# Optimization experiments

Hardware: AMD Instinct MI355X
Metric: run time of the kernel (lower is better)

## Reference

```python
import jax, jax.numpy as jnp
import numpy as np

B = 65536

def setup_inputs() -> dict:
    key = jax.random.key(0)
    k1, k2 = jax.random.split(key, 2)
    x = jax.random.normal(k1, (B, 1, 28, 28), dtype=jnp.float32)
    # classifier params: Linear(4*14*14 -> 10)
    W = jax.random.normal(k2, (10, 4 * 14 * 14), dtype=jnp.float32) * 0.03
    b = jnp.zeros((10,), dtype=jnp.float32)
    return {"x": x, "W": W, "b": b}


def reference(x, W, b):
    # x: [B,1,28,28]
    batch = x.shape[0]
    img = x[:, 0]  # [B,28,28]
    # non-overlapping 2x2 patches, row-major over (r,c), flattened row-major
    # within patch -> matches torch's x[:, r:r+2, c:c+2].view(B, -1)
    patches = img.reshape(batch, 14, 2, 14, 2).transpose(0, 1, 3, 2, 4)
    patches = patches.reshape(batch, 196, 4)
    # Exact closed form of the 4-qubit circuit RY(theta_i) on wire i followed
    # by CNOT chain (0->1->2->3) and <Z_k> measurement:
    #   <Z_k> = prod_{j<=k} cos(theta_j)
    ez = jnp.cumprod(jnp.cos(patches), axis=-1)  # [B,196,4]
    feat = ez.reshape(batch, 4 * 14 * 14)  # [B,784]
    logits = feat @ W.T + b  # [B,10]
    return jax.nn.log_softmax(logits, axis=-1)
```

## Files before the change

### kernel.cpp

```cpp
#include <hip/hip_runtime.h>

#define NCLS 10
#define NUM_IMG 65536

__device__ __forceinline__ void async_cp16(const float* g, float* l) {
    __builtin_amdgcn_global_load_lds(
        (const __attribute__((address_space(1))) void*)(g),
        (__attribute__((address_space(3))) void*)(l),
        16, 0, 0);
}

__global__ __launch_bounds__(448, 7) void quanv_logits_kernel(
    const float* __restrict__ x,
    const float* __restrict__ W,
    const float* __restrict__ bias,
    float* __restrict__ out)
{
    __shared__ float4 sb[2][896];

    const int tid  = threadIdx.x;
    const int w    = __builtin_amdgcn_readfirstlane(tid >> 6);
    const int lane = tid & 63;
    const int img0 = blockIdx.x << 6;

    const int s0 = tid, s1 = tid + 448;
    const float* g0 = x + (size_t)(img0 + s0 / 14) * 784 + (s0 % 14) * 4;
    const float* g1 = x + (size_t)(img0 + s1 / 14) * 784 + (s1 % 14) * 4;

    float acc[NCLS];
#pragma unroll
    for (int c = 0; c < NCLS; ++c) acc[c] = 0.0f;

    async_cp16(g0, (float*)&sb[0][s0]);
    async_cp16(g1, (float*)&sb[0][s1]);
    __syncthreads();

#pragma unroll
    for (int rr = 0; rr < 14; ++rr) {
        const int cur = rr & 1, nxt = cur ^ 1;
        if (rr < 13) {
            async_cp16(g0 + (rr + 1) * 56, (float*)&sb[nxt][s0]);
            async_cp16(g1 + (rr + 1) * 56, (float*)&sb[nxt][s1]);
        }

        const float4 t4 = sb[cur][lane * 14 + w];
        const float4 b4 = sb[cur][lane * 14 + w + 7];

        const float e0 = __cosf(t4.x);
        const float e1 = e0 * __cosf(t4.y);
        const float e2 = e1 * __cosf(b4.x);
        const float e3 = e2 * __cosf(b4.y);
        const float f0 = __cosf(t4.z);
        const float f1 = f0 * __cosf(t4.w);
        const float f2 = f1 * __cosf(b4.z);
        const float f3 = f2 * __cosf(b4.w);

        const int P = (rr * 14 + 2 * w) * 4;
#pragma unroll
        for (int c = 0; c < NCLS; ++c) {
            const float4 wa = *reinterpret_cast<const float4*>(&W[c * 784 + P]);
            const float4 wb = *reinterpret_cast<const float4*>(&W[c * 784 + P + 4]);
            float a = acc[c];
            a = fmaf(e0, wa.x, a); a = fmaf(e1, wa.y, a);
            a = fmaf(e2, wa.z, a); a = fmaf(e3, wa.w, a);
            a = fmaf(f0, wb.x, a); a = fmaf(f1, wb.y, a);
            a = fmaf(f2, wb.z, a); a = fmaf(f3, wb.w, a);
            acc[c] = a;
        }
        __syncthreads();
    }

    float* part = (float*)sb;
#pragma unroll
    for (int c = 0; c < NCLS; ++c) part[lane * 71 + w * NCLS + c] = acc[c];
    __syncthreads();

    if (w == 0) {
        float s[NCLS];
#pragma unroll
        for (int c = 0; c < NCLS; ++c) s[c] = bias[c];
        for (int ww = 0; ww < 7; ++ww) {
#pragma unroll
            for (int c = 0; c < NCLS; ++c) s[c] += part[lane * 71 + ww * NCLS + c];
        }
        float m = s[0];
#pragma unroll
        for (int c = 1; c < NCLS; ++c) m = fmaxf(m, s[c]);
        float sum = 0.0f;
#pragma unroll
        for (int c = 0; c < NCLS; ++c) sum += __expf(s[c] - m);
        const float lse = __logf(sum) + m;

        float* o = out + (size_t)(img0 + lane) * NCLS;
#pragma unroll
        for (int c = 0; c < NCLS; c += 2) {
            float2 v;
            v.x = s[c]     - lse;
            v.y = s[c + 1] - lse;
            *reinterpret_cast<float2*>(o + c) = v;
        }
    }
}

extern "C" void kernel_launch(void* const* d_in, const int* in_sizes, int n_in,
                              void* d_out, int out_size, void* d_ws, size_t ws_size,
                              hipStream_t stream) {
    const float* x    = (const float*)d_in[0];
    const float* W    = (const float*)d_in[1];
    const float* bias = (const float*)d_in[2];
    float* out        = (float*)d_out;

    dim3 block(448);
    dim3 grid(NUM_IMG / 64);
    quanv_logits_kernel<<<grid, block, 0, stream>>>(x, W, bias, out);
}
```

Baseline: 309.0 us.

## Compute classifier GEMM with bf16 MFMA instead of scalar FMAs

Replaces the per-thread FP32 FMA loop over 10 classes with 16x16x32 bf16 MFMA instructions. Each wave handles 16 images, and the weights are repacked into bf16 fragments in LDS once per block. Image data is now loaded directly from global memory into registers, replacing the double-buffered async LDS copy and its per-row barriers. This removes most scalar FMA work and barrier overhead. In exchange it pays a per-block weight repack, wastes MFMA columns on padding, and lowers precision to bf16.

```diff
diff --git a/kernel.cpp b/kernel.cpp
--- a/kernel.cpp
+++ b/kernel.cpp
@@ -1,88 +1,120 @@
 #include <hip/hip_runtime.h>
+#include <hip/hip_bf16.h>
 
 #define NCLS 10
 #define NUM_IMG 65536
 
-__device__ __forceinline__ void async_cp16(const float* g, float* l) {
-    __builtin_amdgcn_global_load_lds(
-        (const __attribute__((address_space(1))) void*)(g),
-        (__attribute__((address_space(3))) void*)(l),
-        16, 0, 0);
+typedef __attribute__((ext_vector_type(8))) short short8;
+typedef __attribute__((ext_vector_type(4))) float f32x4;
+
+union FragAB { short8 v; unsigned int u[4]; };
+
+__device__ __forceinline__ unsigned int pack_bf16(float a, float b) {
+    union { __hip_bfloat162 h; unsigned int u; } cv;
+    cv.h = __float22bfloat162_rn(make_float2(a, b));
+    return cv.u;
 }
 
-__global__ __launch_bounds__(448, 7) void quanv_logits_kernel(
+__global__ __launch_bounds__(256, 4) void quanv_mfma_kernel(
     const float* __restrict__ x,
     const float* __restrict__ W,
     const float* __restrict__ bias,
     float* __restrict__ out)
 {
-    __shared__ float4 sb[2][896];
+    __shared__ unsigned int sWB[28 * 64 * 4];
+    __shared__ float part[4 * 16 * 18];
 
     const int tid  = threadIdx.x;
-    const int w    = __builtin_amdgcn_readfirstlane(tid >> 6);
+    const int wv   = tid >> 6;
     const int lane = tid & 63;
+    const int q    = lane >> 4;
+    const int sub  = lane & 15;
     const int img0 = blockIdx.x << 6;
 
-    const int s0 = tid, s1 = tid + 448;
-    const float* g0 = x + (size_t)(img0 + s0 / 14) * 784 + (s0 % 14) * 4;
-    const float* g1 = x + (size_t)(img0 + s1 / 14) * 784 + (s1 % 14) * 4;
+    for (int f = tid; f < 28 * 64; f += 256) {
+        const int step = f >> 6, sl = f & 63;
+        const int qB = sl >> 4, n = sl & 15;
+        const int rr = step >> 1, h = step & 1;
+        unsigned int u0 = 0, u1 = 0, u2 = 0, u3 = 0;
+        if (n < NCLS) {
+            const int pr0 = 8 * h + 2 * qB;
+            if (pr0 < 14) {
+                const float* wp = W + n * 784 + (rr * 14 + pr0) * 4;
+                u0 = pack_bf16(wp[0], wp[1]);
+                u1 = pack_bf16(wp[2], wp[3]);
+            }
+            if (pr0 + 1 < 14) {
+                const float* wp = W + n * 784 + (rr * 14 + pr0 + 1) * 4;
+                u2 = pack_bf16(wp[0], wp[1]);
+                u3 = pack_bf16(wp[2], wp[3]);
+            }
+        }
+        *reinterpret_cast<uint4*>(&sWB[f * 4]) = make_uint4(u0, u1, u2, u3);
+    }
+    __syncthreads();
 
-    float acc[NCLS];
-#pragma unroll
-    for (int c = 0; c < NCLS; ++c) acc[c] = 0.0f;
-
-    async_cp16(g0, (float*)&sb[0][s0]);
-    async_cp16(g1, (float*)&sb[0][s1]);
-    __syncthreads();
+    const float* __restrict__ img = x + (size_t)(img0 + wv * 16 + sub) * 784;
+    f32x4 acc = {0.f, 0.f, 0.f, 0.f};
 
 #pragma unroll
     for (int rr = 0; rr < 14; ++rr) {
-        const int cur = rr & 1, nxt = cur ^ 1;
-        if (rr < 13) {
-            async_cp16(g0 + (rr + 1) * 56, (float*)&sb[nxt][s0]);
-            async_cp16(g1 + (rr + 1) * 56, (float*)&sb[nxt][s1]);
+        {
+            const float4 t4 = *reinterpret_cast<const float4*>(img + rr * 56 + q * 4);
+            const float4 b4 = *reinterpret_cast<const float4*>(img + rr * 56 + 28 + q * 4);
+            const float e0 = __cosf(t4.x);
+            const float e1 = e0 * __cosf(t4.y);
+            const float e2 = e1 * __cosf(b4.x);
+            const float e3 = e2 * __cosf(b4.y);
+            const float f0 = __cosf(t4.z);
+            const float f1 = f0 * __cosf(t4.w);
+            const float f2 = f1 * __cosf(b4.z);
+            const float f3 = f2 * __cosf(b4.w);
+            FragAB a;
+            a.u[0] = pack_bf16(e0, e1); a.u[1] = pack_bf16(e2, e3);
+            a.u[2] = pack_bf16(f0, f1); a.u[3] = pack_bf16(f2, f3);
+            FragAB bfr;
+            *reinterpret_cast<uint4*>(bfr.u) =
+                *reinterpret_cast<const uint4*>(&sWB[((rr * 2) * 64 + lane) * 4]);
+            acc = __builtin_amdgcn_mfma_f32_16x16x32_bf16(a.v, bfr.v, acc, 0, 0, 0);
         }
-
-        const float4 t4 = sb[cur][lane * 14 + w];
-        const float4 b4 = sb[cur][lane * 14 + w + 7];
-
-        const float e0 = __cosf(t4.x);
-        const float e1 = e0 * __cosf(t4.y);
-        const float e2 = e1 * __cosf(b4.x);
-        const float e3 = e2 * __cosf(b4.y);
-        const float f0 = __cosf(t4.z);
-        const float f1 = f0 * __cosf(t4.w);
-        const float f2 = f1 * __cosf(b4.z);
-        const float f3 = f2 * __cosf(b4.w);
-
-        const int P = (rr * 14 + 2 * w) * 4;
-#pragma unroll
-        for (int c = 0; c < NCLS; ++c) {
-            const float4 wa = *reinterpret_cast<const float4*>(&W[c * 784 + P]);
-            const float4 wb = *reinterpret_cast<const float4*>(&W[c * 784 + P + 4]);
-            float a = acc[c];
-            a = fmaf(e0, wa.x, a); a = fmaf(e1, wa.y, a);
-            a = fmaf(e2, wa.z, a); a = fmaf(e3, wa.w, a);
-            a = fmaf(f0, wb.x, a); a = fmaf(f1, wb.y, a);
-            a = fmaf(f2, wb.z, a); a = fmaf(f3, wb.w, a);
-            acc[c] = a;
+        {
+            float4 t4 = {0.f, 0.f, 0.f, 0.f}, b4 = {0.f, 0.f, 0.f, 0.f};
+            if (q < 3) {
+                t4 = *reinterpret_cast<const float4*>(img + rr * 56 + 16 + q * 4);
+                b4 = *reinterpret_cast<const float4*>(img + rr * 56 + 44 + q * 4);
+            }
+            const float e0 = __cosf(t4.x);
+            const float e1 = e0 * __cosf(t4.y);
+            const float e2 = e1 * __cosf(b4.x);
+            const float e3 = e2 * __cosf(b4.y);
+            const float f0 = __cosf(t4.z);
+            const float f1 = f0 * __cosf(t4.w);
+            const float f2 = f1 * __cosf(b4.z);
+            const float f3 = f2 * __cosf(b4.w);
+            FragAB a;
+            a.u[0] = pack_bf16(e0, e1); a.u[1] = pack_bf16(e2, e3);
+            a.u[2] = pack_bf16(f0, f1); a.u[3] = pack_bf16(f2, f3);
+            FragAB bfr;
+            *reinterpret_cast<uint4*>(bfr.u) =
+                *reinterpret_cast<const uint4*>(&sWB[((rr * 2 + 1) * 64 + lane) * 4]);
+            acc = __builtin_amdgcn_mfma_f32_16x16x32_bf16(a.v, bfr.v, acc, 0, 0, 0);
         }
-        __syncthreads();
     }
 
-    float* part = (float*)sb;
+    float* pw = part + wv * (16 * 18);
+    if (sub < NCLS) {
+        const float bn = bias[sub];
 #pragma unroll
-    for (int c = 0; c < NCLS; ++c) part[lane * 71 + w * NCLS + c] = acc[c];
+        for (int r = 0; r < 4; ++r)
+            pw[(q * 4 + r) * 18 + sub] = acc[r] + bn;
+    }
     __syncthreads();
 
-    if (w == 0) {
+    if (lane < 16) {
+        const float* row = pw + lane * 18;
         float s[NCLS];
 #pragma unroll
-        for (int c = 0; c < NCLS; ++c) s[c] = bias[c];
-        for (int ww = 0; ww < 7; ++ww) {
-#pragma unroll
-            for (int c = 0; c < NCLS; ++c) s[c] += part[lane * 71 + ww * NCLS + c];
-        }
+        for (int c = 0; c < NCLS; ++c) s[c] = row[c];
         float m = s[0];
 #pragma unroll
         for (int c = 1; c < NCLS; ++c) m = fmaxf(m, s[c]);
@@ -91,7 +123,7 @@
         for (int c = 0; c < NCLS; ++c) sum += __expf(s[c] - m);
         const float lse = __logf(sum) + m;
 
-        float* o = out + (size_t)(img0 + lane) * NCLS;
+        float* o = out + (size_t)(img0 + wv * 16 + lane) * NCLS;
 #pragma unroll
         for (int c = 0; c < NCLS; c += 2) {
             float2 v;
@@ -110,7 +142,7 @@
     const float* bias = (const float*)d_in[2];
     float* out        = (float*)d_out;
 
-    dim3 block(448);
+    dim3 block(256);
     dim3 grid(NUM_IMG / 64);
-    quanv_logits_kernel<<<grid, block, 0, stream>>>(x, W, bias, out);
+    quanv_mfma_kernel<<<grid, block, 0, stream>>>(x, W, bias, out);
 }
```

After: 291.0 us. 1.06x faster.
